# Kernel tuning notes

Measured on AMD Instinct MI355X. Metric: run time of the kernel, lower is better.

## Reference

```python
import jax, jax.numpy as jnp
import numpy as np

LATENT_PACKET_SIZE = 16

def setup_inputs() -> dict:
    key = jax.random.key(0)
    z = jax.random.normal(key, (4096, 1, 8192), dtype=jnp.float32)
    return {"z": z}

def reference(z) -> jnp.ndarray:
    B = z.shape[0]
    D = z.shape[2]
    P = LATENT_PACKET_SIZE
    n_packets = D // P
    zp = z.reshape(B, n_packets, P)                      # (B, N, P)
    # sort packets within each sample by the first element of each packet
    inds = jnp.argsort(zp[:, :, 0], axis=1)              # (B, N) int
    z_ordered = jnp.take_along_axis(zp, inds[:, :, None], axis=1)  # batched gather
    return z_ordered.reshape(B, 1, n_packets * P)
```

## Files before the change

### kernel.cpp

```cpp
#include <hip/hip_runtime.h>


#define NPK 512
#define DIM 8192
#define NT  256

__global__ __launch_bounds__(NT, 4)
void sort_latent_kernel(const float* __restrict__ z, float* __restrict__ out) {
    __shared__ float4 row4[DIM / 4];
    __shared__ float  keys[NPK];
    __shared__ int    idxs[NPK];

    const int t = threadIdx.x;
    const size_t rowoff = (size_t)blockIdx.x * DIM;
    const float4* __restrict__ zin4 = (const float4*)(z + rowoff);
    float4* __restrict__ out4 = (float4*)(out + rowoff);

#pragma unroll
    for (int i = 0; i < DIM / 4 / NT; ++i)
        row4[t + NT * i] = zin4[t + NT * i];
    __syncthreads();

    const float* rowf = (const float*)row4;
    keys[t]      = rowf[t * 16];
    keys[t + NT] = rowf[(t + NT) * 16];
    idxs[t]      = t;
    idxs[t + NT] = t + NT;
    __syncthreads();

    for (int k = 2; k <= NPK; k <<= 1) {
        for (int j = k >> 1; j > 0; j >>= 1) {
            const int i = ((t & ~(j - 1)) << 1) | (t & (j - 1));
            const int p = i | j;
            const bool up = ((i & k) == 0);
            const float ka = keys[i], kb = keys[p];
            const int   ia = idxs[i], ib = idxs[p];
            const bool agtb = (ka > kb) || (ka == kb && ia > ib);
            if (agtb == up) {
                keys[i] = kb; keys[p] = ka;
                idxs[i] = ib; idxs[p] = ia;
            }
            __syncthreads();
        }
    }

#pragma unroll
    for (int i = 0; i < DIM / 4 / NT; ++i) {
        const int o = t + NT * i;
        const int src = idxs[o >> 2];
        out4[o] = row4[(src << 2) | (o & 3)];
    }
}

extern "C" void kernel_launch(void* const* d_in, const int* in_sizes, int n_in,
                              void* d_out, int out_size, void* d_ws, size_t ws_size,
                              hipStream_t stream) {
    const float* z = (const float*)d_in[0];
    float* out = (float*)d_out;
    const int nrows = in_sizes[0] / DIM;
    sort_latent_kernel<<<nrows, NT, 0, stream>>>(z, out);
}
```

Before: 231.6 us.

## Replace bitonic sort with rank-counting sort using packed 64-bit keys

Swaps the 45-stage bitonic sort network, which needs a barrier after every stage, for a rank-by-counting scheme. Each of 512 threads compares its packed key (an order-preserving float transform with the index in the low bits) against all 512 keys and scatters its index to the resulting rank. The block size doubles to 512 threads, and shared-memory row storage is XOR-swizzled to cut bank conflicts on the gather. The trade is O(N^2) comparisons per row in exchange for removing the many synchronisations, with a single barrier after key construction.

```diff
diff --git a/kernel.cpp b/kernel.cpp
--- a/kernel.cpp
+++ b/kernel.cpp
@@ -3,13 +3,15 @@
 
 #define NPK 512
 #define DIM 8192
-#define NT  256
+#define NT  512
 
-__global__ __launch_bounds__(NT, 4)
+__device__ __forceinline__ int swz(int e) { return e ^ ((e >> 3) & 7); }
+
+__global__ __launch_bounds__(NT, 8)
 void sort_latent_kernel(const float* __restrict__ z, float* __restrict__ out) {
     __shared__ float4 row4[DIM / 4];
-    __shared__ float  keys[NPK];
-    __shared__ int    idxs[NPK];
+    __shared__ __align__(16) unsigned long long keys[NPK];
+    __shared__ int srcs[NPK];
 
     const int t = threadIdx.x;
     const size_t rowoff = (size_t)blockIdx.x * DIM;
@@ -17,38 +19,38 @@
     float4* __restrict__ out4 = (float4*)(out + rowoff);
 
 #pragma unroll
-    for (int i = 0; i < DIM / 4 / NT; ++i)
-        row4[t + NT * i] = zin4[t + NT * i];
+    for (int i = 0; i < DIM / 4 / NT; ++i) {
+        const int e = t + NT * i;
+        const float4 v = zin4[e];
+        row4[swz(e)] = v;
+        if ((t & 3) == 0) {
+            const int p = (t >> 2) + (NT / 4) * i;
+            unsigned int u = __float_as_uint(v.x);
+            if (u == 0x80000000u) u = 0u;
+            u = (u & 0x80000000u) ? ~u : (u | 0x80000000u);
+            keys[p] = ((unsigned long long)u << 16) | (unsigned long long)p;
+        }
+    }
     __syncthreads();
 
-    const float* rowf = (const float*)row4;
-    keys[t]      = rowf[t * 16];
-    keys[t + NT] = rowf[(t + NT) * 16];
-    idxs[t]      = t;
-    idxs[t + NT] = t + NT;
+    const unsigned long long k0 = keys[t];
+    const ulonglong2* kv = (const ulonglong2*)keys;
+    int r0 = 0;
+#pragma unroll 8
+    for (int j = 0; j < NPK / 2; j += 2) {
+        const ulonglong2 a = kv[j];
+        const ulonglong2 b = kv[j + 1];
+        r0 += (int)(a.x < k0) + (int)(a.y < k0)
+            + (int)(b.x < k0) + (int)(b.y < k0);
+    }
+    srcs[r0] = t;
     __syncthreads();
-
-    for (int k = 2; k <= NPK; k <<= 1) {
-        for (int j = k >> 1; j > 0; j >>= 1) {
-            const int i = ((t & ~(j - 1)) << 1) | (t & (j - 1));
-            const int p = i | j;
-            const bool up = ((i & k) == 0);
-            const float ka = keys[i], kb = keys[p];
-            const int   ia = idxs[i], ib = idxs[p];
-            const bool agtb = (ka > kb) || (ka == kb && ia > ib);
-            if (agtb == up) {
-                keys[i] = kb; keys[p] = ka;
-                idxs[i] = ib; idxs[p] = ia;
-            }
-            __syncthreads();
-        }
-    }
 
 #pragma unroll
     for (int i = 0; i < DIM / 4 / NT; ++i) {
         const int o = t + NT * i;
-        const int src = idxs[o >> 2];
-        out4[o] = row4[(src << 2) | (o & 3)];
+        const int src = srcs[o >> 2];
+        out4[o] = row4[swz((src << 2) | (o & 3))];
     }
 }
 
```

After: 243.9 us. +5.3%, slower.
